# Kernel tuning notes

Hardware: AMD Instinct MI355X
Metric: run time of the kernel (lower is better)

## Reference

```python
import jax, jax.numpy as jnp
import numpy as np


def sine_encode_2d(pos, d):
    # pos: (..., 2) normalized relative positions in [-1, 1]; output (..., d)
    # standard sinusoidal encoding per coordinate, d/2 dims each (sin/cos pairs)
    d_half = d // 2
    n_freq = d_half // 2
    freqs = jnp.exp(-jnp.log(jnp.float32(10000.0)) * jnp.arange(n_freq, dtype=jnp.float32) / n_freq)
    parts = []
    for i in range(2):
        ang = pos[..., i:i + 1] * freqs  # (..., n_freq)
        parts.append(jnp.sin(ang))
        parts.append(jnp.cos(ang))
    return jnp.concatenate(parts, axis=-1)


def rpe_bias(W_rpe, t_q, f_q, t_k, f_k, N_t, N_f, d_rpe):
    dt_norm = jnp.arange(-(N_t - 1), N_t, dtype=jnp.float32) / max(N_t - 1, 1)
    df_norm = jnp.arange(-(N_f - 1), N_f, dtype=jnp.float32) / max(N_f - 1, 1)
    DT, DF = jnp.meshgrid(dt_norm, df_norm, indexing='ij')       # (2Nt-1, 2Nf-1)
    rel = jnp.stack([DT, DF], axis=-1)                            # (2Nt-1, 2Nf-1, 2)
    enc = sine_encode_2d(rel, d_rpe)                              # (2Nt-1, 2Nf-1, d_rpe)
    table = enc @ W_rpe.T                                         # (2Nt-1, 2Nf-1, h)
    n_df = 2 * N_f - 1
    flat = table.reshape(-1, table.shape[-1])                     # ((2Nt-1)*(2Nf-1), h)
    dt_idx = t_q[:, None] - t_k[None, :] + (N_t - 1)              # (Nq, Nk)
    df_idx = f_q[:, None] - f_k[None, :] + (N_f - 1)
    flat_idx = jnp.clip(dt_idx * n_df + df_idx, 0, flat.shape[0] - 1)
    bias = flat[flat_idx]                                         # (Nq, Nk, h)
    return jnp.transpose(bias, (2, 0, 1))                         # (h, Nq, Nk)


def setup_inputs() -> dict:
    key = jax.random.key(0)
    ks = jax.random.split(key, 12)
    B, N_t, N_f, d_model, n_heads, d_rpe = 8, 14, 72, 256, 8, 32
    N = N_t * N_f
    s = 1.0 / np.sqrt(d_model)
    return {
        'q_tokens': jax.random.normal(ks[0], (B, N, d_model), jnp.float32),
        'k_tokens': jax.random.normal(ks[1], (B, N, d_model), jnp.float32),
        'v_tokens': jax.random.normal(ks[2], (B, N, d_model), jnp.float32),
        't_q': jax.random.randint(ks[3], (N,), 0, N_t),
        'f_q': jax.random.randint(ks[4], (N,), 0, N_f),
        't_k': jax.random.randint(ks[5], (N,), 0, N_t),
        'f_k': jax.random.randint(ks[6], (N,), 0, N_f),
        'N_t': N_t,
        'N_f': N_f,
        'W_q': jax.random.normal(ks[7], (d_model, d_model), jnp.float32) * s,
        'W_k': jax.random.normal(ks[8], (d_model, d_model), jnp.float32) * s,
        'W_v': jax.random.normal(ks[9], (d_model, d_model), jnp.float32) * s,
        'W_o': jax.random.normal(ks[10], (d_model, d_model), jnp.float32) * s,
        'W_rpe': jax.random.normal(ks[11], (n_heads, d_rpe), jnp.float32) * (1.0 / np.sqrt(d_rpe)),
    }


def reference(q_tokens, k_tokens, v_tokens, t_q, f_q, t_k, f_k, N_t, N_f,
              W_q, W_k, W_v, W_o, W_rpe):
    B, N_q, d_model = q_tokens.shape
    N_k = k_tokens.shape[1]
    h = W_rpe.shape[0]
    d_rpe = W_rpe.shape[1]
    dk = d_model // h
    scale = jnp.float32(np.sqrt(dk))
    Q = (q_tokens @ W_q.T).reshape(B, N_q, h, dk)
    K = (k_tokens @ W_k.T).reshape(B, N_k, h, dk)
    V = (v_tokens @ W_v.T).reshape(B, N_k, h, dk)
    scores = jnp.einsum('bqhd,bkhd->bhqk', Q, K) / scale          # (B, h, Nq, Nk)
    bias = rpe_bias(W_rpe, t_q, f_q, t_k, f_k, N_t, N_f, d_rpe)   # (h, Nq, Nk)
    attn = jax.nn.softmax(scores + bias[None], axis=-1)
    out = jnp.einsum('bhqk,bkhd->bqhd', attn, V).reshape(B, N_q, d_model)
    return out @ W_o.T
```

## Files before the change

### kernel.cpp

```cpp
#include <hip/hip_runtime.h>

#define B_    8
#define N_    1008
#define D_    256
#define H_    8
#define DK_   32
#define DA_   64
#define BND_  (B_*N_*D_)

typedef _Float16 half8_t __attribute__((ext_vector_type(8)));
typedef _Float16 half4_t __attribute__((ext_vector_type(4)));
typedef float    f32x4   __attribute__((ext_vector_type(4)));

__global__ void prep_kernel(const int* __restrict__ t_q, const int* __restrict__ f_q,
                            const int* __restrict__ t_k, const int* __restrict__ f_k,
                            const float* __restrict__ W_rpe,
                            _Float16* __restrict__ Qa, _Float16* __restrict__ Ka)
{
    const float FR[8] = {1.f, 0.31622776601683794f, 0.1f, 0.03162277660168379f,
                         0.01f, 0.0031622776601683794f, 0.001f, 0.00031622776601683794f};
    int id = blockIdx.x * 256 + threadIdx.x;
    if (id < N_ * H_) {
        int q = id >> 3, h = id & 7;
        float tq = (float)t_q[q] * (1.f / 13.f);
        float fq = (float)f_q[q] * (1.f / 71.f);
        const float* Wh = W_rpe + h * 32;
        half8_t u0, u1, u2, u3;
#pragma unroll
        for (int i = 0; i < 8; i++) {
            float sa = sinf(tq * FR[i]), ca = cosf(tq * FR[i]);
            float sb = sinf(fq * FR[i]), cb = cosf(fq * FR[i]);
            u0[i] = (_Float16)(Wh[i] * sa + Wh[8 + i] * ca);
            u1[i] = (_Float16)(Wh[8 + i] * sa - Wh[i] * ca);
            u2[i] = (_Float16)(Wh[16 + i] * sb + Wh[24 + i] * cb);
            u3[i] = (_Float16)(Wh[24 + i] * sb - Wh[16 + i] * cb);
        }
#pragma unroll
        for (int b = 0; b < 8; b++) {
            _Float16* dst = &Qa[(((size_t)(b * 8 + h)) * N_ + q) * DA_ + 32];
            *(half8_t*)(dst + 0) = u0;  *(half8_t*)(dst + 8) = u1;
            *(half8_t*)(dst + 16) = u2; *(half8_t*)(dst + 24) = u3;
        }
    } else if (id < N_ * H_ + N_ * 64) {
        int id2 = id - N_ * H_;
        int k = id2 >> 6, bh = id2 & 63;
        float tk = (float)t_k[k] * (1.f / 13.f);
        float fk = (float)f_k[k] * (1.f / 71.f);
        half8_t v0, v1, v2, v3;
#pragma unroll
        for (int i = 0; i < 8; i++) {
            v0[i] = (_Float16)cosf(tk * FR[i]);
            v1[i] = (_Float16)sinf(tk * FR[i]);
            v2[i] = (_Float16)cosf(fk * FR[i]);
            v3[i] = (_Float16)sinf(fk * FR[i]);
        }
        _Float16* dst = &Ka[(((size_t)bh) * N_ + k) * DA_ + 32];
        *(half8_t*)(dst + 0) = v0;  *(half8_t*)(dst + 8) = v1;
        *(half8_t*)(dst + 16) = v2; *(half8_t*)(dst + 24) = v3;
    }
}

__global__ __launch_bounds__(256, 2) void qkv_gemm(
    const float* __restrict__ q_tok, const float* __restrict__ k_tok,
    const float* __restrict__ v_tok, const float* __restrict__ Wq,
    const float* __restrict__ Wk, const float* __restrict__ Wv,
    _Float16* __restrict__ Qa, _Float16* __restrict__ Ka, _Float16* __restrict__ Vt)
{
    __shared__ __align__(16) _Float16 fw[8 * 8 * 64 * 8];
    const int tid = threadIdx.x;
    const int lane = tid & 63, w = tid >> 6, quad = lane >> 4, l15 = lane & 15;
    const int z = blockIdx.z;
    const int m0 = blockIdx.x * 128, n0 = blockIdx.y * 128;
    const float* A = (z == 0) ? q_tok : (z == 1) ? k_tok : v_tok;
    const float* W = (z == 0) ? Wq : (z == 1) ? Wk : Wv;

#pragma unroll
    for (int p = 0; p < 16; p++) {
        int g = p * 256 + tid;
        int ch = g >> 9, rem = g & 511, nt = rem >> 6, L = rem & 63;
        const float* src = &W[(size_t)(n0 + nt * 16 + (L & 15)) * D_ + ch * 32 + ((L >> 4) & 3) * 8];
        float4 w0 = *(const float4*)src;
        float4 w1 = *(const float4*)(src + 4);
        half8_t hv = {(_Float16)w0.x, (_Float16)w0.y, (_Float16)w0.z, (_Float16)w0.w,
                      (_Float16)w1.x, (_Float16)w1.y, (_Float16)w1.z, (_Float16)w1.w};
        *(half8_t*)&fw[g * 8] = hv;
    }
    __syncthreads();

    f32x4 acc[2][8] = {};
    const float* Ar0 = &A[(size_t)(m0 + w * 16 + l15) * D_];
    const float* Ar1 = Ar0 + (size_t)64 * D_;
#pragma unroll
    for (int ch = 0; ch < 8; ch++) {
        float4 a00 = *(const float4*)&Ar0[ch * 32 + quad * 8];
        float4 a01 = *(const float4*)&Ar0[ch * 32 + quad * 8 + 4];
        float4 a10 = *(const float4*)&Ar1[ch * 32 + quad * 8];
        float4 a11 = *(const float4*)&Ar1[ch * 32 + quad * 8 + 4];
        half8_t af0 = {(_Float16)a00.x, (_Float16)a00.y, (_Float16)a00.z, (_Float16)a00.w,
                       (_Float16)a01.x, (_Float16)a01.y, (_Float16)a01.z, (_Float16)a01.w};
        half8_t af1 = {(_Float16)a10.x, (_Float16)a10.y, (_Float16)a10.z, (_Float16)a10.w,
                       (_Float16)a11.x, (_Float16)a11.y, (_Float16)a11.z, (_Float16)a11.w};
#pragma unroll
        for (int nt = 0; nt < 8; nt++) {
            half8_t bf = *(const half8_t*)&fw[((ch * 8 + nt) * 64 + lane) * 8];
            acc[0][nt] = __builtin_amdgcn_mfma_f32_16x16x32_f16(af0, bf, acc[0][nt], 0, 0, 0);
            acc[1][nt] = __builtin_amdgcn_mfma_f32_16x16x32_f16(af1, bf, acc[1][nt], 0, 0, 0);
        }
    }
    const float scale = (z == 0) ? 0.17677669529663687f : 1.0f;
#pragma unroll
    for (int mt = 0; mt < 2; mt++) {
        int mbase = m0 + mt * 64 + w * 16 + quad * 4;
        int b = mbase / N_;
        int q = mbase - b * N_;
        if (z < 2) {
            _Float16* out = (z == 0) ? Qa : Ka;
#pragma unroll
            for (int nt = 0; nt < 8; nt++) {
                int n = n0 + nt * 16 + l15;
                int hh = n >> 5, d = n & 31;
                _Float16* dst = &out[(((size_t)(b * 8 + hh)) * N_ + q) * DA_ + d];
#pragma unroll
                for (int r = 0; r < 4; r++)
                    dst[(size_t)r * DA_] = (_Float16)(acc[mt][nt][r] * scale);
            }
        } else {
#pragma unroll
            for (int nt = 0; nt < 8; nt++) {
                int n = n0 + nt * 16 + l15;
                int hh = n >> 5, d = n & 31;
                half4_t o = {(_Float16)acc[mt][nt][0], (_Float16)acc[mt][nt][1],
                             (_Float16)acc[mt][nt][2], (_Float16)acc[mt][nt][3]};
                *(half4_t*)&Vt[(((size_t)(b * 8 + hh)) * DK_ + d) * N_ + q] = o;
            }
        }
    }
}

__global__ __launch_bounds__(256, 2) void attn(const _Float16* __restrict__ Qa,
    const _Float16* __restrict__ Ka, const _Float16* __restrict__ Vt,
    _Float16* __restrict__ AO)
{
    __shared__ __align__(16) _Float16 fk[2][4096];
    __shared__ __align__(16) _Float16 fv[2][2048];
    __shared__ __align__(16) _Float16 plds[4][2][16][72];

    const int tid = threadIdx.x;
    const int lane = tid & 63, w = tid >> 6, quad = lane >> 4, l15 = lane & 15;
    const int bh = blockIdx.y, q0 = blockIdx.x * 128;
    const int b = bh >> 3, hh = bh & 7;
    const _Float16* Kb = Ka + (size_t)bh * N_ * DA_;
    const _Float16* Vb = Vt + (size_t)bh * DK_ * N_;

    const int s_l15 = tid & 15, s_quad = (tid >> 4) & 3;
    const int s_mt = tid >> 6;
    const int s_c = tid >> 7;
    const int s_mt2 = (tid >> 6) & 1;

    half8_t qf[2][2];
    int qg[2];
#pragma unroll
    for (int g = 0; g < 2; g++) {
        qg[g] = q0 + w * 32 + g * 16 + l15;
        int qc = qg[g] < N_ ? qg[g] : N_ - 1;
        const _Float16* Qrow = &Qa[((size_t)bh * N_ + qc) * DA_];
        qf[g][0] = *(const half8_t*)&Qrow[quad * 8];
        qf[g][1] = *(const half8_t*)&Qrow[32 + quad * 8];
    }

    float m_run[2] = {-1e30f, -1e30f}, l_run[2] = {0.f, 0.f};
    f32x4 O[2][2] = {};

    {
        int krow = s_mt * 16 + s_l15;
        *(half8_t*)&fk[0][((s_mt * 2 + 0) * 64 + lane) * 8] =
            *(const half8_t*)&Kb[(size_t)krow * DA_ + s_quad * 8];
        *(half8_t*)&fk[0][((s_mt * 2 + 1) * 64 + lane) * 8] =
            *(const half8_t*)&Kb[(size_t)krow * DA_ + 32 + s_quad * 8];
        int vrow = s_mt2 * 16 + s_l15;
        int vcol = s_c * 32 + s_quad * 8;
        *(half8_t*)&fv[0][tid * 8] = *(const half8_t*)&Vb[(size_t)vrow * N_ + vcol];
    }
    __syncthreads();

    for (int kt = 0; kt < 16; kt++) {
        const int cb = kt & 1;
        if (kt < 15) {
            int k0n = (kt + 1) * 64;
            int krow = k0n + s_mt * 16 + s_l15;
            if (krow > N_ - 1) krow = N_ - 1;
            *(half8_t*)&fk[cb ^ 1][((s_mt * 2 + 0) * 64 + lane) * 8] =
                *(const half8_t*)&Kb[(size_t)krow * DA_ + s_quad * 8];
            *(half8_t*)&fk[cb ^ 1][((s_mt * 2 + 1) * 64 + lane) * 8] =
                *(const half8_t*)&Kb[(size_t)krow * DA_ + 32 + s_quad * 8];
            int vrow = s_mt2 * 16 + s_l15;
            int vcol = k0n + s_c * 32 + s_quad * 8;
            if (vcol > N_ - 8) vcol = N_ - 8;
            *(half8_t*)&fv[cb ^ 1][tid * 8] = *(const half8_t*)&Vb[(size_t)vrow * N_ + vcol];
        }
        half8_t kf[4][2], vf[4];
#pragma unroll
        for (int mt = 0; mt < 4; mt++) {
            kf[mt][0] = *(const half8_t*)&fk[cb][((mt * 2 + 0) * 64 + lane) * 8];
            kf[mt][1] = *(const half8_t*)&fk[cb][((mt * 2 + 1) * 64 + lane) * 8];
        }
#pragma unroll
        for (int f2 = 0; f2 < 4; f2++)
            vf[f2] = *(const half8_t*)&fv[cb][(f2 * 64 + lane) * 8];

#pragma unroll
        for (int g = 0; g < 2; g++) {
            f32x4 S[4];
#pragma unroll
            for (int mt = 0; mt < 4; mt++) {
                f32x4 zz = {0.f, 0.f, 0.f, 0.f};
                zz = __builtin_amdgcn_mfma_f32_16x16x32_f16(kf[mt][0], qf[g][0], zz, 0, 0, 0);
                S[mt] = __builtin_amdgcn_mfma_f32_16x16x32_f16(kf[mt][1], qf[g][1], zz, 0, 0, 0);
            }
            if (kt == 15)
                S[3] = (f32x4){-1e30f, -1e30f, -1e30f, -1e30f};
            float tmax = -1e30f;
#pragma unroll
            for (int mt = 0; mt < 4; mt++)
#pragma unroll
                for (int r = 0; r < 4; r++) tmax = fmaxf(tmax, S[mt][r]);
            tmax = fmaxf(tmax, __shfl_xor(tmax, 16, 64));
            tmax = fmaxf(tmax, __shfl_xor(tmax, 32, 64));
            float mnew = fmaxf(m_run[g], tmax);
            float alpha = __expf(m_run[g] - mnew);
            m_run[g] = mnew;
            float tsum = 0.f;
#pragma unroll
            for (int mt = 0; mt < 4; mt++) {
                float p0 = __expf(S[mt][0] - mnew), p1 = __expf(S[mt][1] - mnew);
                float p2 = __expf(S[mt][2] - mnew), p3 = __expf(S[mt][3] - mnew);
                tsum += (p0 + p1) + (p2 + p3);
                half4_t ph = {(_Float16)p0, (_Float16)p1, (_Float16)p2, (_Float16)p3};
                *(half4_t*)&plds[w][g][l15][mt * 16 + quad * 4] = ph;
            }
            tsum += __shfl_xor(tsum, 16, 64);
            tsum += __shfl_xor(tsum, 32, 64);
            l_run[g] = l_run[g] * alpha + tsum;
            O[g][0] = O[g][0] * alpha;
            O[g][1] = O[g][1] * alpha;
        }
#pragma unroll
        for (int g = 0; g < 2; g++) {
#pragma unroll
            for (int c = 0; c < 2; c++) {
                half8_t pf = *(const half8_t*)&plds[w][g][l15][c * 32 + quad * 8];
                O[g][0] = __builtin_amdgcn_mfma_f32_16x16x32_f16(vf[c * 2 + 0], pf, O[g][0], 0, 0, 0);
                O[g][1] = __builtin_amdgcn_mfma_f32_16x16x32_f16(vf[c * 2 + 1], pf, O[g][1], 0, 0, 0);
            }
        }
        __syncthreads();
    }
#pragma unroll
    for (int g = 0; g < 2; g++) {
        if (qg[g] < N_) {
            float inv = 1.f / l_run[g];
#pragma unroll
            for (int mt2 = 0; mt2 < 2; mt2++) {
                half4_t o = {(_Float16)(O[g][mt2][0] * inv), (_Float16)(O[g][mt2][1] * inv),
                             (_Float16)(O[g][mt2][2] * inv), (_Float16)(O[g][mt2][3] * inv)};
                *(half4_t*)&AO[((size_t)b * N_ + qg[g]) * D_ + hh * DK_ + mt2 * 16 + quad * 4] = o;
            }
        }
    }
}

__global__ __launch_bounds__(256, 2) void out_gemm(const _Float16* __restrict__ A,
    const float* __restrict__ W, float* __restrict__ out)
{
    __shared__ __align__(16) _Float16 fw[8 * 8 * 64 * 8];
    const int tid = threadIdx.x;
    const int lane = tid & 63, w = tid >> 6, quad = lane >> 4, l15 = lane & 15;
    const int m0 = blockIdx.x * 128, n0 = blockIdx.y * 128;

#pragma unroll
    for (int p = 0; p < 16; p++) {
        int g = p * 256 + tid;
        int ch = g >> 9, rem = g & 511, nt = rem >> 6, L = rem & 63;
        const float* src = &W[(size_t)(n0 + nt * 16 + (L & 15)) * D_ + ch * 32 + ((L >> 4) & 3) * 8];
        float4 w0 = *(const float4*)src;
        float4 w1 = *(const float4*)(src + 4);
        half8_t hv = {(_Float16)w0.x, (_Float16)w0.y, (_Float16)w0.z, (_Float16)w0.w,
                      (_Float16)w1.x, (_Float16)w1.y, (_Float16)w1.z, (_Float16)w1.w};
        *(half8_t*)&fw[g * 8] = hv;
    }
    __syncthreads();

    f32x4 acc[2][8] = {};
    const _Float16* Ar0 = &A[(size_t)(m0 + w * 16 + l15) * D_];
    const _Float16* Ar1 = Ar0 + (size_t)64 * D_;
#pragma unroll
    for (int ch = 0; ch < 8; ch++) {
        half8_t af0 = *(const half8_t*)&Ar0[ch * 32 + quad * 8];
        half8_t af1 = *(const half8_t*)&Ar1[ch * 32 + quad * 8];
#pragma unroll
        for (int nt = 0; nt < 8; nt++) {
            half8_t bf = *(const half8_t*)&fw[((ch * 8 + nt) * 64 + lane) * 8];
            acc[0][nt] = __builtin_amdgcn_mfma_f32_16x16x32_f16(af0, bf, acc[0][nt], 0, 0, 0);
            acc[1][nt] = __builtin_amdgcn_mfma_f32_16x16x32_f16(af1, bf, acc[1][nt], 0, 0, 0);
        }
    }
#pragma unroll
    for (int mt = 0; mt < 2; mt++) {
        int mbase = m0 + mt * 64 + w * 16 + quad * 4;
#pragma unroll
        for (int nt = 0; nt < 8; nt++) {
            int n = n0 + nt * 16 + l15;
#pragma unroll
            for (int r = 0; r < 4; r++)
                out[(size_t)(mbase + r) * D_ + n] = acc[mt][nt][r];
        }
    }
}

extern "C" void kernel_launch(void* const* d_in, const int* in_sizes, int n_in,
                              void* d_out, int out_size, void* d_ws, size_t ws_size,
                              hipStream_t stream)
{
    const float* q_tokens = (const float*)d_in[0];
    const float* k_tokens = (const float*)d_in[1];
    const float* v_tokens = (const float*)d_in[2];
    const int*   t_q      = (const int*)d_in[3];
    const int*   f_q      = (const int*)d_in[4];
    const int*   t_k      = (const int*)d_in[5];
    const int*   f_k      = (const int*)d_in[6];
    const float* W_q   = (const float*)d_in[9];
    const float* W_k   = (const float*)d_in[10];
    const float* W_v   = (const float*)d_in[11];
    const float* W_o   = (const float*)d_in[12];
    const float* W_rpe = (const float*)d_in[13];

    _Float16* ws = (_Float16*)d_ws;
    _Float16* Qa = ws;
    _Float16* Ka = Qa + (size_t)64 * N_ * DA_;
    _Float16* Vt = Ka + (size_t)64 * N_ * DA_;
    _Float16* AO = Vt + (size_t)64 * DK_ * N_;

    prep_kernel<<<dim3(284), 256, 0, stream>>>(t_q, f_q, t_k, f_k, W_rpe, Qa, Ka);
    qkv_gemm<<<dim3(63, 2, 3), 256, 0, stream>>>(q_tokens, k_tokens, v_tokens,
                                                 W_q, W_k, W_v, Qa, Ka, Vt);
    attn<<<dim3(8, 64), 256, 0, stream>>>(Qa, Ka, Vt, AO);
    out_gemm<<<dim3(63, 2), 256, 0, stream>>>(AO, W_o, (float*)d_out);
}
```

Baseline: 169.5 us.

## Halve attention query tile per block and switch softmax to exp2

The attention kernel now handles 64 queries per block (one 16-row group per wave) instead of 128, doubling the grid to 1024 blocks and raising launch bounds to 4 blocks per CU for more parallelism and occupancy. The log2(e) factor is folded into the Q scale and the RPE query columns so the softmax can use a native exp2 instead of __expf. The cost is that each K/V tile loaded into LDS is now reused by half as many queries, doubling K/V global and LDS traffic.

```diff
diff --git a/kernel.cpp b/kernel.cpp
--- a/kernel.cpp
+++ b/kernel.cpp
@@ -7,10 +7,21 @@
 #define DK_   32
 #define DA_   64
 #define BND_  (B_*N_*D_)
+#define L2E_  1.4426950408889634f
 
 typedef _Float16 half8_t __attribute__((ext_vector_type(8)));
 typedef _Float16 half4_t __attribute__((ext_vector_type(4)));
 typedef float    f32x4   __attribute__((ext_vector_type(4)));
+
+#if defined(__has_builtin)
+#if __has_builtin(__builtin_amdgcn_exp2f)
+#define EXP2(x) __builtin_amdgcn_exp2f(x)
+#else
+#define EXP2(x) exp2f(x)
+#endif
+#else
+#define EXP2(x) exp2f(x)
+#endif
 
 __global__ void prep_kernel(const int* __restrict__ t_q, const int* __restrict__ f_q,
                             const int* __restrict__ t_k, const int* __restrict__ f_k,
@@ -30,10 +41,10 @@
         for (int i = 0; i < 8; i++) {
             float sa = sinf(tq * FR[i]), ca = cosf(tq * FR[i]);
             float sb = sinf(fq * FR[i]), cb = cosf(fq * FR[i]);
-            u0[i] = (_Float16)(Wh[i] * sa + Wh[8 + i] * ca);
-            u1[i] = (_Float16)(Wh[8 + i] * sa - Wh[i] * ca);
-            u2[i] = (_Float16)(Wh[16 + i] * sb + Wh[24 + i] * cb);
-            u3[i] = (_Float16)(Wh[24 + i] * sb - Wh[16 + i] * cb);
+            u0[i] = (_Float16)(L2E_ * (Wh[i] * sa + Wh[8 + i] * ca));
+            u1[i] = (_Float16)(L2E_ * (Wh[8 + i] * sa - Wh[i] * ca));
+            u2[i] = (_Float16)(L2E_ * (Wh[16 + i] * sb + Wh[24 + i] * cb));
+            u3[i] = (_Float16)(L2E_ * (Wh[24 + i] * sb - Wh[16 + i] * cb));
         }
 #pragma unroll
         for (int b = 0; b < 8; b++) {
@@ -107,7 +118,7 @@
             acc[1][nt] = __builtin_amdgcn_mfma_f32_16x16x32_f16(af1, bf, acc[1][nt], 0, 0, 0);
         }
     }
-    const float scale = (z == 0) ? 0.17677669529663687f : 1.0f;
+    const float scale = (z == 0) ? 0.17677669529663687f * L2E_ : 1.0f;
 #pragma unroll
     for (int mt = 0; mt < 2; mt++) {
         int mbase = m0 + mt * 64 + w * 16 + quad * 4;
@@ -137,17 +148,17 @@
     }
 }
 
-__global__ __launch_bounds__(256, 2) void attn(const _Float16* __restrict__ Qa,
+__global__ __launch_bounds__(256, 4) void attn(const _Float16* __restrict__ Qa,
     const _Float16* __restrict__ Ka, const _Float16* __restrict__ Vt,
     _Float16* __restrict__ AO)
 {
     __shared__ __align__(16) _Float16 fk[2][4096];
     __shared__ __align__(16) _Float16 fv[2][2048];
-    __shared__ __align__(16) _Float16 plds[4][2][16][72];
+    __shared__ __align__(16) _Float16 plds[4][16][72];
 
     const int tid = threadIdx.x;
     const int lane = tid & 63, w = tid >> 6, quad = lane >> 4, l15 = lane & 15;
-    const int bh = blockIdx.y, q0 = blockIdx.x * 128;
+    const int bh = blockIdx.y, q0 = blockIdx.x * 64;
     const int b = bh >> 3, hh = bh & 7;
     const _Float16* Kb = Ka + (size_t)bh * N_ * DA_;
     const _Float16* Vb = Vt + (size_t)bh * DK_ * N_;
@@ -157,19 +168,14 @@
     const int s_c = tid >> 7;
     const int s_mt2 = (tid >> 6) & 1;
 
-    half8_t qf[2][2];
-    int qg[2];
-#pragma unroll
-    for (int g = 0; g < 2; g++) {
-        qg[g] = q0 + w * 32 + g * 16 + l15;
-        int qc = qg[g] < N_ ? qg[g] : N_ - 1;
-        const _Float16* Qrow = &Qa[((size_t)bh * N_ + qc) * DA_];
-        qf[g][0] = *(const half8_t*)&Qrow[quad * 8];
-        qf[g][1] = *(const half8_t*)&Qrow[32 + quad * 8];
-    }
-
-    float m_run[2] = {-1e30f, -1e30f}, l_run[2] = {0.f, 0.f};
-    f32x4 O[2][2] = {};
+    const int qg = q0 + w * 16 + l15;
+    const int qc = qg < N_ ? qg : N_ - 1;
+    const _Float16* Qrow = &Qa[((size_t)bh * N_ + qc) * DA_];
+    half8_t qf0 = *(const half8_t*)&Qrow[quad * 8];
+    half8_t qf1 = *(const half8_t*)&Qrow[32 + quad * 8];
+
+    float m_run = -1e30f, l_run = 0.f;
+    f32x4 O[2] = {};
 
     {
         int krow = s_mt * 16 + s_l15;
@@ -198,73 +204,58 @@
             if (vcol > N_ - 8) vcol = N_ - 8;
             *(half8_t*)&fv[cb ^ 1][tid * 8] = *(const half8_t*)&Vb[(size_t)vrow * N_ + vcol];
         }
-        half8_t kf[4][2], vf[4];
+        f32x4 S[4];
 #pragma unroll
         for (int mt = 0; mt < 4; mt++) {
-            kf[mt][0] = *(const half8_t*)&fk[cb][((mt * 2 + 0) * 64 + lane) * 8];
-            kf[mt][1] = *(const half8_t*)&fk[cb][((mt * 2 + 1) * 64 + lane) * 8];
-        }
-#pragma unroll
-        for (int f2 = 0; f2 < 4; f2++)
-            vf[f2] = *(const half8_t*)&fv[cb][(f2 * 64 + lane) * 8];
-
-#pragma unroll
-        for (int g = 0; g < 2; g++) {
-            f32x4 S[4];
-#pragma unroll
-            for (int mt = 0; mt < 4; mt++) {
-                f32x4 zz = {0.f, 0.f, 0.f, 0.f};
-                zz = __builtin_amdgcn_mfma_f32_16x16x32_f16(kf[mt][0], qf[g][0], zz, 0, 0, 0);
-                S[mt] = __builtin_amdgcn_mfma_f32_16x16x32_f16(kf[mt][1], qf[g][1], zz, 0, 0, 0);
-            }
-            if (kt == 15)
-                S[3] = (f32x4){-1e30f, -1e30f, -1e30f, -1e30f};
-            float tmax = -1e30f;
-#pragma unroll
-            for (int mt = 0; mt < 4; mt++)
-#pragma unroll
-                for (int r = 0; r < 4; r++) tmax = fmaxf(tmax, S[mt][r]);
-            tmax = fmaxf(tmax, __shfl_xor(tmax, 16, 64));
-            tmax = fmaxf(tmax, __shfl_xor(tmax, 32, 64));
-            float mnew = fmaxf(m_run[g], tmax);
-            float alpha = __expf(m_run[g] - mnew);
-            m_run[g] = mnew;
-            float tsum = 0.f;
-#pragma unroll
-            for (int mt = 0; mt < 4; mt++) {
-                float p0 = __expf(S[mt][0] - mnew), p1 = __expf(S[mt][1] - mnew);
-                float p2 = __expf(S[mt][2] - mnew), p3 = __expf(S[mt][3] - mnew);
-                tsum += (p0 + p1) + (p2 + p3);
-                half4_t ph = {(_Float16)p0, (_Float16)p1, (_Float16)p2, (_Float16)p3};
-                *(half4_t*)&plds[w][g][l15][mt * 16 + quad * 4] = ph;
-            }
-            tsum += __shfl_xor(tsum, 16, 64);
-            tsum += __shfl_xor(tsum, 32, 64);
-            l_run[g] = l_run[g] * alpha + tsum;
-            O[g][0] = O[g][0] * alpha;
-            O[g][1] = O[g][1] * alpha;
-        }
-#pragma unroll
-        for (int g = 0; g < 2; g++) {
-#pragma unroll
-            for (int c = 0; c < 2; c++) {
-                half8_t pf = *(const half8_t*)&plds[w][g][l15][c * 32 + quad * 8];
-                O[g][0] = __builtin_amdgcn_mfma_f32_16x16x32_f16(vf[c * 2 + 0], pf, O[g][0], 0, 0, 0);
-                O[g][1] = __builtin_amdgcn_mfma_f32_16x16x32_f16(vf[c * 2 + 1], pf, O[g][1], 0, 0, 0);
-            }
+            half8_t kf0 = *(const half8_t*)&fk[cb][((mt * 2 + 0) * 64 + lane) * 8];
+            half8_t kf1 = *(const half8_t*)&fk[cb][((mt * 2 + 1) * 64 + lane) * 8];
+            f32x4 zz = {0.f, 0.f, 0.f, 0.f};
+            zz = __builtin_amdgcn_mfma_f32_16x16x32_f16(kf0, qf0, zz, 0, 0, 0);
+            S[mt] = __builtin_amdgcn_mfma_f32_16x16x32_f16(kf1, qf1, zz, 0, 0, 0);
+        }
+        if (kt == 15)
+            S[3] = (f32x4){-1e30f, -1e30f, -1e30f, -1e30f};
+        float tmax = -1e30f;
+#pragma unroll
+        for (int mt = 0; mt < 4; mt++)
+#pragma unroll
+            for (int r = 0; r < 4; r++) tmax = fmaxf(tmax, S[mt][r]);
+        tmax = fmaxf(tmax, __shfl_xor(tmax, 16, 64));
+        tmax = fmaxf(tmax, __shfl_xor(tmax, 32, 64));
+        float mnew = fmaxf(m_run, tmax);
+        float alpha = EXP2(m_run - mnew);
+        m_run = mnew;
+        float tsum = 0.f;
+#pragma unroll
+        for (int mt = 0; mt < 4; mt++) {
+            float p0 = EXP2(S[mt][0] - mnew), p1 = EXP2(S[mt][1] - mnew);
+            float p2 = EXP2(S[mt][2] - mnew), p3 = EXP2(S[mt][3] - mnew);
+            tsum += (p0 + p1) + (p2 + p3);
+            half4_t ph = {(_Float16)p0, (_Float16)p1, (_Float16)p2, (_Float16)p3};
+            *(half4_t*)&plds[w][l15][mt * 16 + quad * 4] = ph;
+        }
+        tsum += __shfl_xor(tsum, 16, 64);
+        tsum += __shfl_xor(tsum, 32, 64);
+        l_run = l_run * alpha + tsum;
+        O[0] = O[0] * alpha;
+        O[1] = O[1] * alpha;
+#pragma unroll
+        for (int c = 0; c < 2; c++) {
+            half8_t pf = *(const half8_t*)&plds[w][l15][c * 32 + quad * 8];
+            half8_t vfa = *(const half8_t*)&fv[cb][((c * 2 + 0) * 64 + lane) * 8];
+            half8_t vfb = *(const half8_t*)&fv[cb][((c * 2 + 1) * 64 + lane) * 8];
+            O[0] = __builtin_amdgcn_mfma_f32_16x16x32_f16(vfa, pf, O[0], 0, 0, 0);
+            O[1] = __builtin_amdgcn_mfma_f32_16x16x32_f16(vfb, pf, O[1], 0, 0, 0);
         }
         __syncthreads();
     }
-#pragma unroll
-    for (int g = 0; g < 2; g++) {
-        if (qg[g] < N_) {
-            float inv = 1.f / l_run[g];
-#pragma unroll
-            for (int mt2 = 0; mt2 < 2; mt2++) {
-                half4_t o = {(_Float16)(O[g][mt2][0] * inv), (_Float16)(O[g][mt2][1] * inv),
-                             (_Float16)(O[g][mt2][2] * inv), (_Float16)(O[g][mt2][3] * inv)};
-                *(half4_t*)&AO[((size_t)b * N_ + qg[g]) * D_ + hh * DK_ + mt2 * 16 + quad * 4] = o;
-            }
+    if (qg < N_) {
+        float inv = 1.f / l_run;
+#pragma unroll
+        for (int mt2 = 0; mt2 < 2; mt2++) {
+            half4_t o = {(_Float16)(O[mt2][0] * inv), (_Float16)(O[mt2][1] * inv),
+                         (_Float16)(O[mt2][2] * inv), (_Float16)(O[mt2][3] * inv)};
+            *(half4_t*)&AO[((size_t)b * N_ + qg) * D_ + hh * DK_ + mt2 * 16 + quad * 4] = o;
         }
     }
 }
@@ -343,6 +334,6 @@
     prep_kernel<<<dim3(284), 256, 0, stream>>>(t_q, f_q, t_k, f_k, W_rpe, Qa, Ka);
     qkv_gemm<<<dim3(63, 2, 3), 256, 0, stream>>>(q_tokens, k_tokens, v_tokens,
                                                  W_q, W_k, W_v, Qa, Ka, Vt);
-    attn<<<dim3(8, 64), 256, 0, stream>>>(Qa, Ka, Vt, AO);
+    attn<<<dim3(16, 64), 256, 0, stream>>>(Qa, Ka, Vt, AO);
     out_gemm<<<dim3(63, 2), 256, 0, stream>>>(AO, W_o, (float*)d_out);
 }
```

New measurement: 162.1 us. -4.3%, faster.
